# Performance work log

Measured on AMD Instinct MI355X. Metric: run time of the kernel, lower is better.

Reference implementation:

```python
import jax, jax.numpy as jnp
import numpy as np

NEG_SLOPE = 0.01  # nn.LeakyReLU default used in module

def leaky_relu(x):
    return jnp.where(x >= 0, x, NEG_SLOPE * x)

def setup_inputs() -> dict:
    key = jax.random.key(0)
    k1, k2, k3, k4, k5 = jax.random.split(key, 5)
    B, S, D, H, E = 4, 2048, 1024, 2048, 8
    s_in = 1.0 / np.sqrt(D)
    return {
        "inputs": jax.random.normal(k1, (B, S, D), dtype=jnp.float32),
        "Wg": jax.random.normal(k2, (E, D), dtype=jnp.float32) * s_in,
        "bg": jax.random.normal(k3, (E,), dtype=jnp.float32) * s_in,
        "We": jax.random.normal(k4, (E, H, D), dtype=jnp.float32) * s_in,
        "be": jax.random.normal(k5, (E, H), dtype=jnp.float32) * s_in,
    }

def reference(inputs, Wg, bg, We, be):
    # gate: [B,S,E]
    gate_logits = jnp.einsum('bsd,ed->bse', inputs, Wg) + bg
    gate_probs = jax.nn.softmax(gate_logits, axis=-1)
    # all experts densely: [B,S,E,H]
    expert_out = leaky_relu(jnp.einsum('bsd,ehd->bseh', inputs, We) + be)
    # gate-weighted reduction over experts: [B,S,H]
    weighted = jnp.einsum('bseh,bse->bsh', expert_out, gate_probs)
    return weighted
```

## Files before the change

kernel.cpp:

```cpp
#include <hip/hip_runtime.h>
#include <hip/hip_bf16.h>
#include <math.h>

#define M_TOK 8192
#define N_H   2048
#define K_D   1024
#define N_E   8

typedef __bf16 bf16x8 __attribute__((ext_vector_type(8)));
typedef __bf16 bf16x4 __attribute__((ext_vector_type(4)));
typedef float  f32x4  __attribute__((ext_vector_type(4)));

__device__ inline f32x4 mfma16(bf16x8 a, bf16x8 b, f32x4 c) {
  return __builtin_amdgcn_mfma_f32_16x16x32_bf16(a, b, c, 0, 0, 0);
}

__device__ inline void load16_lds(const void* g, void* l) {
  __builtin_amdgcn_global_load_lds(
      (const __attribute__((address_space(1))) void*)g,
      (__attribute__((address_space(3))) void*)l, 16, 0, 0);
}

__global__ __launch_bounds__(256) void cvt_kernel(const float* __restrict__ src,
                                                  __bf16* __restrict__ dst,
                                                  int n4) {
  int i = blockIdx.x * blockDim.x + threadIdx.x;
  const int stride = gridDim.x * blockDim.x;
  for (; i < n4; i += stride) {
    float4 v = ((const float4*)src)[i];
    bf16x4 o = {(__bf16)v.x, (__bf16)v.y, (__bf16)v.z, (__bf16)v.w};
    *(bf16x4*)(dst + (size_t)i * 4) = o;
  }
}

__global__ __launch_bounds__(256) void gate_kernel(const float* __restrict__ X,
                                                   const float* __restrict__ Wg,
                                                   const float* __restrict__ bg,
                                                   float* __restrict__ gate,
                                                   __bf16* __restrict__ Xb) {
  const int tid = threadIdx.x;
  const int lane = tid & 63;
  const int wv = tid >> 6;
  const int token = blockIdx.x * 4 + wv;
  const float* xrow = X + (size_t)token * K_D;

  float xr[16];
#pragma unroll
  for (int i = 0; i < 16; ++i) xr[i] = xrow[lane + i * 64];

#pragma unroll
  for (int i = 0; i < 16; ++i)
    Xb[(size_t)token * K_D + lane + i * 64] = (__bf16)xr[i];

  float l[N_E];
#pragma unroll
  for (int e = 0; e < N_E; ++e) {
    const float* wrow = Wg + e * K_D;
    float s = 0.f;
#pragma unroll
    for (int i = 0; i < 16; ++i) s += xr[i] * wrow[lane + i * 64];
#pragma unroll
    for (int off = 32; off > 0; off >>= 1) s += __shfl_xor(s, off);
    l[e] = s + bg[e];
  }
  float mx = l[0];
#pragma unroll
  for (int e = 1; e < N_E; ++e) mx = fmaxf(mx, l[e]);
  float p[N_E], den = 0.f;
#pragma unroll
  for (int e = 0; e < N_E; ++e) { p[e] = expf(l[e] - mx); den += p[e]; }
  const float inv = 1.f / den;
  if (lane == 0) {
#pragma unroll
    for (int e = 0; e < N_E; ++e) gate[(size_t)token * N_E + e] = p[e] * inv;
  }
}

__global__ __launch_bounds__(256, 2) void moe_main(
    const __bf16* __restrict__ Xb, const __bf16* __restrict__ Wb,
    const float* __restrict__ gate, const float* __restrict__ be,
    float* __restrict__ out) {
  __shared__ __bf16 As[2][128 * 32];
  __shared__ __bf16 Bs[2][256 * 32];
  __shared__ float gS[128 * 8];
  __shared__ float bS[8 * 128];

  const int tid = threadIdx.x;
  const int lane = tid & 63;
  const int wv = tid >> 6;
  const int wr = wv >> 1, wn = wv & 1;
  const int row0 = blockIdx.x * 128;
  const int col0 = blockIdx.y * 128;

  for (int i = tid; i < 1024; i += 256) {
    gS[i] = gate[(size_t)row0 * N_E + i];
    bS[i] = be[(size_t)(i >> 7) * N_H + col0 + (i & 127)];
  }

  const int rA = tid >> 2;
  const int kk = (tid & 3) * 8;
  const __bf16* aB = Xb + (size_t)(row0 + rA) * K_D + kk;
  const __bf16* bB = Wb + (size_t)(col0 + rA) * K_D + kk;

  const int lr = lane & 15;
  const int lk = (lane >> 4) * 8;
  const __bf16* aRd0 = &As[0][(wr * 64 + lr) * 32 + lk];
  const __bf16* aRd1 = &As[1][(wr * 64 + lr) * 32 + lk];
  const __bf16* bRd0 = &Bs[0][(wn * 64 + lr) * 32 + lk];
  const __bf16* bRd1 = &Bs[1][(wn * 64 + lr) * 32 + lk];

  f32x4 fin[4][4];
#pragma unroll
  for (int m = 0; m < 4; ++m)
#pragma unroll
    for (int h = 0; h < 4; ++h) fin[m][h] = (f32x4){0.f, 0.f, 0.f, 0.f};

  f32x4 acc[4][8];
#pragma unroll
  for (int m = 0; m < 4; ++m)
#pragma unroll
    for (int n = 0; n < 8; ++n) acc[m][n] = (f32x4){0.f, 0.f, 0.f, 0.f};

  auto STAGE = [&](int tn, int bufN) {
    const int k0 = (tn & 31) << 5;
    const size_t pOff = (size_t)(tn >> 5) << 22;
    const __bf16* a = aB + k0;
    load16_lds(a, &As[bufN][wv * 512]);
    load16_lds(a + (size_t)64 * K_D, &As[bufN][2048 + wv * 512]);
    const __bf16* b = bB + pOff + k0;
    load16_lds(b, &Bs[bufN][wv * 512]);
    load16_lds(b + (size_t)64 * K_D, &Bs[bufN][2048 + wv * 512]);
    load16_lds(b + (size_t)N_H * K_D, &Bs[bufN][4096 + wv * 512]);
    load16_lds(b + (size_t)(N_H + 64) * K_D, &Bs[bufN][6144 + wv * 512]);
  };

  auto EPI = [&](int p) {
    const int e0 = p * 2;
#pragma unroll
    for (int m = 0; m < 4; ++m) {
#pragma unroll
      for (int j = 0; j < 4; ++j) {
        const int r = wr * 64 + m * 16 + (lane >> 4) * 4 + j;
        const float g0 = gS[r * 8 + e0];
        const float g1 = gS[r * 8 + e0 + 1];
#pragma unroll
        for (int h = 0; h < 4; ++h) {
          const int c = wn * 64 + h * 16 + lr;
          float v0 = acc[m][h][j] + bS[e0 * 128 + c];
          v0 = (v0 >= 0.f) ? v0 : 0.01f * v0;
          float v1 = acc[m][4 + h][j] + bS[(e0 + 1) * 128 + c];
          v1 = (v1 >= 0.f) ? v1 : 0.01f * v1;
          fin[m][h][j] += g0 * v0 + g1 * v1;
        }
      }
    }
#pragma unroll
    for (int m = 0; m < 4; ++m)
#pragma unroll
      for (int n = 0; n < 8; ++n) acc[m][n] = (f32x4){0.f, 0.f, 0.f, 0.f};
  };

  auto STEP = [&](int t, const __bf16* aRd, const __bf16* bRd, int bufN,
                  bool doStage, bool lastStep) {
    if (lastStep)
      asm volatile("s_waitcnt vmcnt(0)" ::: "memory");
    else
      asm volatile("s_waitcnt vmcnt(6)" ::: "memory");
    __builtin_amdgcn_s_barrier();
    __builtin_amdgcn_sched_barrier(0);

    __builtin_amdgcn_s_setprio(1);
    bf16x8 af[4], bfr[8];
#pragma unroll
    for (int m = 0; m < 4; ++m) af[m] = *(const bf16x8*)(aRd + m * 512);
#pragma unroll
    for (int n = 0; n < 8; ++n)
      bfr[n] = *(const bf16x8*)(bRd + ((n >> 2) * 128 + (n & 3) * 16) * 32);
#pragma unroll
    for (int n = 0; n < 8; ++n)
#pragma unroll
      for (int m = 0; m < 4; ++m)
        acc[m][n] = mfma16(af[m], bfr[n], acc[m][n]);
    __builtin_amdgcn_s_setprio(0);

    asm volatile("s_waitcnt lgkmcnt(0)" ::: "memory");
    __builtin_amdgcn_s_barrier();

    if (doStage) STAGE(t + 2, bufN);
    if ((t & 31) == 31) EPI(t >> 5);
  };

  STAGE(0, 0);
  STAGE(1, 1);

#pragma unroll 1
  for (int t2 = 0; t2 < 126; t2 += 2) {
    STEP(t2 + 0, aRd0, bRd0, 0, true, false);
    STEP(t2 + 1, aRd1, bRd1, 1, true, false);
  }
  STEP(126, aRd0, bRd0, 0, false, false);
  STEP(127, aRd1, bRd1, 1, false, true);

#pragma unroll
  for (int m = 0; m < 4; ++m) {
#pragma unroll
    for (int j = 0; j < 4; ++j) {
      const size_t r = (size_t)(row0 + wr * 64 + m * 16 + (lane >> 4) * 4 + j);
#pragma unroll
      for (int h = 0; h < 4; ++h) {
        out[r * N_H + col0 + wn * 64 + h * 16 + lr] = fin[m][h][j];
      }
    }
  }
}

extern "C" void kernel_launch(void* const* d_in, const int* in_sizes, int n_in,
                              void* d_out, int out_size, void* d_ws, size_t ws_size,
                              hipStream_t stream) {
  const float* X  = (const float*)d_in[0];
  const float* Wg = (const float*)d_in[1];
  const float* bg = (const float*)d_in[2];
  const float* We = (const float*)d_in[3];
  const float* be = (const float*)d_in[4];
  float* out = (float*)d_out;

  char* ws = (char*)d_ws;
  __bf16* Xb   = (__bf16*)(ws);
  __bf16* Wb   = (__bf16*)(ws + (size_t)16 * 1024 * 1024);
  float*  gate = (float*)(ws + (size_t)48 * 1024 * 1024);

  cvt_kernel<<<2048, 256, 0, stream>>>(We, Wb, (N_E * N_H * K_D) / 4);

  gate_kernel<<<M_TOK / 4, 256, 0, stream>>>(X, Wg, bg, gate, Xb);

  dim3 grid(M_TOK / 128, N_H / 128);
  moe_main<<<grid, 256, 0, stream>>>(Xb, Wb, gate, be, out);
}
```

Measured before the change: 320.0 us.

## Merge gate and weight conversion kernels; issue next-stage loads before MFMAs

Folds the expert-weight fp32-to-bf16 conversion into the gate kernel as extra blocks, which removes one launch and lets both preprocessing jobs run concurrently. In the main GEMM loop, the LDS fragment reads are now waited on and followed by a barrier before the MFMAs, and the next stage's global-to-LDS loads are issued ahead of the MFMA block rather than after it. This lets memory traffic overlap the matrix math and drops the trailing barrier. The cost is extra VGPR pressure from keeping fragments live across the barrier. The conversion indexing also assumes a fixed grid size (2048 blocks × 256 threads × 8 iterations).

```diff
diff --git a/kernel.cpp b/kernel.cpp
--- a/kernel.cpp
+++ b/kernel.cpp
@@ -21,27 +21,29 @@
       (__attribute__((address_space(3))) void*)l, 16, 0, 0);
 }
 
-__global__ __launch_bounds__(256) void cvt_kernel(const float* __restrict__ src,
-                                                  __bf16* __restrict__ dst,
-                                                  int n4) {
-  int i = blockIdx.x * blockDim.x + threadIdx.x;
-  const int stride = gridDim.x * blockDim.x;
-  for (; i < n4; i += stride) {
-    float4 v = ((const float4*)src)[i];
-    bf16x4 o = {(__bf16)v.x, (__bf16)v.y, (__bf16)v.z, (__bf16)v.w};
-    *(bf16x4*)(dst + (size_t)i * 4) = o;
-  }
-}
-
-__global__ __launch_bounds__(256) void gate_kernel(const float* __restrict__ X,
-                                                   const float* __restrict__ Wg,
-                                                   const float* __restrict__ bg,
-                                                   float* __restrict__ gate,
-                                                   __bf16* __restrict__ Xb) {
+__global__ __launch_bounds__(256) void gate_cvt_kernel(
+    const float* __restrict__ X, const float* __restrict__ Wg,
+    const float* __restrict__ bg, const float* __restrict__ We,
+    float* __restrict__ gate, __bf16* __restrict__ Xb,
+    __bf16* __restrict__ Wb) {
+  const int blk = blockIdx.x;
+  if (blk >= 2048) {
+    const int base = (blk - 2048) * 256 + threadIdx.x;
+    const float4* src = (const float4*)We;
+#pragma unroll
+    for (int i = 0; i < 8; ++i) {
+      const int idx = base + i * 524288;
+      float4 v = src[idx];
+      bf16x4 o = {(__bf16)v.x, (__bf16)v.y, (__bf16)v.z, (__bf16)v.w};
+      *(bf16x4*)(Wb + (size_t)idx * 4) = o;
+    }
+    return;
+  }
+
   const int tid = threadIdx.x;
   const int lane = tid & 63;
   const int wv = tid >> 6;
-  const int token = blockIdx.x * 4 + wv;
+  const int token = blk * 4 + wv;
   const float* xrow = X + (size_t)token * K_D;
 
   float xr[16];
@@ -167,15 +169,20 @@
     else
       asm volatile("s_waitcnt vmcnt(6)" ::: "memory");
     __builtin_amdgcn_s_barrier();
-    __builtin_amdgcn_sched_barrier(0);
-
-    __builtin_amdgcn_s_setprio(1);
+
     bf16x8 af[4], bfr[8];
 #pragma unroll
     for (int m = 0; m < 4; ++m) af[m] = *(const bf16x8*)(aRd + m * 512);
 #pragma unroll
     for (int n = 0; n < 8; ++n)
       bfr[n] = *(const bf16x8*)(bRd + ((n >> 2) * 128 + (n & 3) * 16) * 32);
+    asm volatile("s_waitcnt lgkmcnt(0)" ::: "memory");
+    __builtin_amdgcn_sched_barrier(0);
+    __builtin_amdgcn_s_barrier();
+
+    if (doStage) STAGE(t + 2, bufN);
+
+    __builtin_amdgcn_s_setprio(1);
 #pragma unroll
     for (int n = 0; n < 8; ++n)
 #pragma unroll
@@ -183,10 +190,6 @@
         acc[m][n] = mfma16(af[m], bfr[n], acc[m][n]);
     __builtin_amdgcn_s_setprio(0);
 
-    asm volatile("s_waitcnt lgkmcnt(0)" ::: "memory");
-    __builtin_amdgcn_s_barrier();
-
-    if (doStage) STAGE(t + 2, bufN);
     if ((t & 31) == 31) EPI(t >> 5);
   };
 
@@ -229,9 +232,7 @@
   __bf16* Wb   = (__bf16*)(ws + (size_t)16 * 1024 * 1024);
   float*  gate = (float*)(ws + (size_t)48 * 1024 * 1024);
 
-  cvt_kernel<<<2048, 256, 0, stream>>>(We, Wb, (N_E * N_H * K_D) / 4);
-
-  gate_kernel<<<M_TOK / 4, 256, 0, stream>>>(X, Wg, bg, gate, Xb);
+  gate_cvt_kernel<<<4096, 256, 0, stream>>>(X, Wg, bg, We, gate, Xb, Wb);
 
   dim3 grid(M_TOK / 128, N_H / 128);
   moe_main<<<grid, 256, 0, stream>>>(Xb, Wb, gate, be, out);
```

Measured after the change: 321.6 us. No clear change (+0.5%).

## Enlarge MoE GEMM tile to 256 rows with a 4-deep LDS ring buffer

Applied to the files above, without the earlier changes.

Doubles the block to 512 threads so each block covers 256 tokens by 128 hidden columns for an expert pair. Shared memory grows from a double buffer to a 4-slot ring, and the next stage's global-to-LDS load is issued right after this phase's fragment reads. This removes the second barrier per k-step and improves B-operand reuse across more rows. In exchange, LDS use rises to about 140KB, which likely allows only one block per CU. The launch bound of two 512-thread blocks may also force register pressure or spills.

```diff
diff --git a/kernel.cpp b/kernel.cpp
--- a/kernel.cpp
+++ b/kernel.cpp
@@ -76,26 +76,26 @@
   }
 }
 
-__global__ __launch_bounds__(256, 2) void moe_main(
+__global__ __launch_bounds__(512, 2) void moe_main(
     const __bf16* __restrict__ Xb, const __bf16* __restrict__ Wb,
     const float* __restrict__ gate, const float* __restrict__ be,
     float* __restrict__ out) {
-  __shared__ __bf16 As[2][128 * 32];
-  __shared__ __bf16 Bs[2][256 * 32];
-  __shared__ float gS[128 * 8];
+  __shared__ __bf16 As[4][8192];
+  __shared__ __bf16 Bs[4][8192];
+  __shared__ float gS[256 * 8];
   __shared__ float bS[8 * 128];
 
   const int tid = threadIdx.x;
   const int lane = tid & 63;
   const int wv = tid >> 6;
-  const int wr = wv >> 1, wn = wv & 1;
-  const int row0 = blockIdx.x * 128;
+  const int wm = wv >> 1;
+  const int wn = wv & 1;
+  const int row0 = blockIdx.x * 256;
   const int col0 = blockIdx.y * 128;
 
-  for (int i = tid; i < 1024; i += 256) {
-    gS[i] = gate[(size_t)row0 * N_E + i];
+  for (int i = tid; i < 2048; i += 512) gS[i] = gate[(size_t)row0 * N_E + i];
+  for (int i = tid; i < 1024; i += 512)
     bS[i] = be[(size_t)(i >> 7) * N_H + col0 + (i & 127)];
-  }
 
   const int rA = tid >> 2;
   const int kk = (tid & 3) * 8;
@@ -104,10 +104,8 @@
 
   const int lr = lane & 15;
   const int lk = (lane >> 4) * 8;
-  const __bf16* aRd0 = &As[0][(wr * 64 + lr) * 32 + lk];
-  const __bf16* aRd1 = &As[1][(wr * 64 + lr) * 32 + lk];
-  const __bf16* bRd0 = &Bs[0][(wn * 64 + lr) * 32 + lk];
-  const __bf16* bRd1 = &Bs[1][(wn * 64 + lr) * 32 + lk];
+  const int aOff = (wm * 64 + lr) * 32 + lk;
+  const int bOff = (wn * 64 + lr) * 32 + lk;
 
   f32x4 fin[4][4];
 #pragma unroll
@@ -121,17 +119,13 @@
 #pragma unroll
     for (int n = 0; n < 8; ++n) acc[m][n] = (f32x4){0.f, 0.f, 0.f, 0.f};
 
-  auto STAGE = [&](int tn, int bufN) {
-    const int k0 = (tn & 31) << 5;
-    const size_t pOff = (size_t)(tn >> 5) << 22;
-    const __bf16* a = aB + k0;
-    load16_lds(a, &As[bufN][wv * 512]);
-    load16_lds(a + (size_t)64 * K_D, &As[bufN][2048 + wv * 512]);
-    const __bf16* b = bB + pOff + k0;
-    load16_lds(b, &Bs[bufN][wv * 512]);
-    load16_lds(b + (size_t)64 * K_D, &Bs[bufN][2048 + wv * 512]);
-    load16_lds(b + (size_t)N_H * K_D, &Bs[bufN][4096 + wv * 512]);
-    load16_lds(b + (size_t)(N_H + 64) * K_D, &Bs[bufN][6144 + wv * 512]);
+  auto STAGE = [&](int sn, int q) {
+    const int k0 = (sn & 31) << 5;
+    const size_t pOff = (size_t)(sn >> 5) << 22;
+    load16_lds(aB + k0, &As[q][tid * 8]);
+    load16_lds(aB + (size_t)128 * K_D + k0, &As[q][4096 + tid * 8]);
+    load16_lds(bB + pOff + k0, &Bs[q][tid * 8]);
+    load16_lds(bB + pOff + (size_t)N_H * K_D + k0, &Bs[q][4096 + tid * 8]);
   };
 
   auto EPI = [&](int p) {
@@ -140,7 +134,7 @@
     for (int m = 0; m < 4; ++m) {
 #pragma unroll
       for (int j = 0; j < 4; ++j) {
-        const int r = wr * 64 + m * 16 + (lane >> 4) * 4 + j;
+        const int r = wm * 64 + m * 16 + (lane >> 4) * 4 + j;
         const float g0 = gS[r * 8 + e0];
         const float g1 = gS[r * 8 + e0 + 1];
 #pragma unroll
@@ -160,22 +154,27 @@
       for (int n = 0; n < 8; ++n) acc[m][n] = (f32x4){0.f, 0.f, 0.f, 0.f};
   };
 
-  auto STEP = [&](int t, const __bf16* aRd, const __bf16* bRd, int bufN,
-                  bool doStage, bool lastStep) {
-    if (lastStep)
+  auto PHASE = [&](int sn, int q, bool doStage, bool lastPhase) {
+    if (lastPhase)
       asm volatile("s_waitcnt vmcnt(0)" ::: "memory");
     else
-      asm volatile("s_waitcnt vmcnt(6)" ::: "memory");
+      asm volatile("s_waitcnt vmcnt(4)" ::: "memory");
     __builtin_amdgcn_s_barrier();
     __builtin_amdgcn_sched_barrier(0);
 
+    bf16x8 af[4], bfr[8];
+#pragma unroll
+    for (int m = 0; m < 4; ++m)
+      af[m] = *(const bf16x8*)(&As[q][aOff + m * 512]);
+#pragma unroll
+    for (int n = 0; n < 8; ++n)
+      bfr[n] = *(const bf16x8*)(&Bs[q][bOff + ((n >> 2) * 128 + (n & 3) * 16) * 32]);
+    asm volatile("s_waitcnt lgkmcnt(0)" ::: "memory");
+    __builtin_amdgcn_sched_barrier(0);
+
+    if (doStage) STAGE(sn + 2, (q + 2) & 3);
+
     __builtin_amdgcn_s_setprio(1);
-    bf16x8 af[4], bfr[8];
-#pragma unroll
-    for (int m = 0; m < 4; ++m) af[m] = *(const bf16x8*)(aRd + m * 512);
-#pragma unroll
-    for (int n = 0; n < 8; ++n)
-      bfr[n] = *(const bf16x8*)(bRd + ((n >> 2) * 128 + (n & 3) * 16) * 32);
 #pragma unroll
     for (int n = 0; n < 8; ++n)
 #pragma unroll
@@ -183,29 +182,30 @@
         acc[m][n] = mfma16(af[m], bfr[n], acc[m][n]);
     __builtin_amdgcn_s_setprio(0);
 
-    asm volatile("s_waitcnt lgkmcnt(0)" ::: "memory");
-    __builtin_amdgcn_s_barrier();
-
-    if (doStage) STAGE(t + 2, bufN);
-    if ((t & 31) == 31) EPI(t >> 5);
+    if ((sn & 31) == 31) EPI(sn >> 5);
   };
 
   STAGE(0, 0);
   STAGE(1, 1);
 
 #pragma unroll 1
-  for (int t2 = 0; t2 < 126; t2 += 2) {
-    STEP(t2 + 0, aRd0, bRd0, 0, true, false);
-    STEP(t2 + 1, aRd1, bRd1, 1, true, false);
-  }
-  STEP(126, aRd0, bRd0, 0, false, false);
-  STEP(127, aRd1, bRd1, 1, false, true);
+  for (int t4 = 0; t4 < 31; ++t4) {
+    const int sn = t4 * 4;
+    PHASE(sn + 0, 0, true, false);
+    PHASE(sn + 1, 1, true, false);
+    PHASE(sn + 2, 2, true, false);
+    PHASE(sn + 3, 3, true, false);
+  }
+  PHASE(124, 0, true, false);
+  PHASE(125, 1, true, false);
+  PHASE(126, 2, false, false);
+  PHASE(127, 3, false, true);
 
 #pragma unroll
   for (int m = 0; m < 4; ++m) {
 #pragma unroll
     for (int j = 0; j < 4; ++j) {
-      const size_t r = (size_t)(row0 + wr * 64 + m * 16 + (lane >> 4) * 4 + j);
+      const size_t r = (size_t)(row0 + wm * 64 + m * 16 + (lane >> 4) * 4 + j);
 #pragma unroll
       for (int h = 0; h < 4; ++h) {
         out[r * N_H + col0 + wn * 64 + h * 16 + lr] = fin[m][h][j];
@@ -233,6 +233,6 @@
 
   gate_kernel<<<M_TOK / 4, 256, 0, stream>>>(X, Wg, bg, gate, Xb);
 
-  dim3 grid(M_TOK / 128, N_H / 128);
-  moe_main<<<grid, 256, 0, stream>>>(Xb, Wb, gate, be, out);
-}
+  dim3 grid(M_TOK / 256, N_H / 128);
+  moe_main<<<grid, 512, 0, stream>>>(Xb, Wb, gate, be, out);
+}
```

Result: faster. 304.5 us (median of 3 runs) (-4.8%).
